# Kernel tuning notes

Measured on AMD Instinct MI355X. Metric: run time of the kernel, lower is better.

## Reference

```python
import jax, jax.numpy as jnp
import numpy as np

BIN_SIZE = 128
DIST_MULT = 0.1
CLIP_LOW = 0.0
EPS = 1e-6


def setup_inputs() -> dict:
    key = jax.random.key(0)
    k1, k2, k3, k4 = jax.random.split(key, 4)
    B, N = 8, 25600          # n_points multiple of bin_size=128 -> 200 bins
    D_MSG, D_NODE = 128, 256  # distance_dim, node feature dim
    MAX_BINS = 200
    x_msg = jax.random.normal(k1, (B, N, D_MSG), dtype=jnp.float32)
    x_node = jax.random.normal(k2, (B, N, D_NODE), dtype=jnp.float32)
    msk = jax.random.uniform(k3, (B, N)) < 0.9
    rotations = jax.random.normal(k4, (D_MSG, MAX_BINS // 2), dtype=jnp.float32)
    return {"x_msg": x_msg, "x_node": x_node, "msk": msk, "rotations": rotations}


def reference(x_msg, x_node, msk, rotations):
    B, N, _ = x_msg.shape
    n_bins = N // BIN_SIZE

    # LSH projection and binning
    mul = x_msg @ rotations[:, : max(1, n_bins // 2)]          # (B, N, n_bins/2)
    cmul = jnp.concatenate([mul, -mul], axis=-1)               # (B, N, n_bins)
    bin_idx = jnp.argmax(cmul, axis=-1) + jnp.where(~msk, n_bins - 1, 0)
    bins_split = jnp.argsort(bin_idx, axis=-1).reshape(B, n_bins, BIN_SIZE)

    # gather points into bins (batch_dims=1 gather)
    flat = bins_split.reshape(B, N)
    x_msg_b = jnp.take_along_axis(x_msg, flat[..., None], axis=1).reshape(B, n_bins, BIN_SIZE, -1)
    x_node_b = jnp.take_along_axis(x_node, flat[..., None], axis=1).reshape(B, n_bins, BIN_SIZE, -1)
    msk_f = msk.astype(x_msg.dtype)[..., None]                 # (B, N, 1)
    msk_b = jnp.take_along_axis(msk_f, flat[..., None], axis=1).reshape(B, n_bins, BIN_SIZE, 1)

    # NodePairGaussianKernel (l2 norm) within each bin
    x = x_msg_b * msk_b                                        # (B, nb, P, D)
    sq = jnp.sum(jnp.square(x), axis=-1)                       # (B, nb, P)
    gram = jnp.einsum('bkid,bkjd->bkij', x, x)                 # (B, nb, P, P)
    d = jnp.sqrt(jnp.maximum(sq[..., :, None] - 2.0 * gram + sq[..., None, :], EPS))
    dm = jnp.clip(jnp.exp(-DIST_MULT * d), CLIP_LOW, 1.0)[..., None]  # (B, nb, P, P, 1)

    # mask rows and columns
    dm = dm * msk_b[:, :, :, None, :] * msk_b[:, :, None, :, :]
    return bins_split, x_node_b, dm, msk_b
```

## Files before the change

kernel.cpp:

```cpp
#include <hip/hip_runtime.h>
#include <stdint.h>

typedef unsigned int uint32;

#define B 8
#define N 25600
#define DMSG 128
#define DNODE 256
#define NBINS 200
#define PBIN 128
#define NR 100
#define NPASS 4
#define JPP 25
#define NKEY 400
#define CH 256
#define NCHUNK 100
#define EPS 1e-6f
#define DISTM 0.1f

typedef short short8 __attribute__((ext_vector_type(8)));
typedef float floatx4 __attribute__((ext_vector_type(4)));

__device__ __forceinline__ unsigned short f2bf(float f) {
    uint32 u = __float_as_uint(f);
    u += 0x7fffu + ((u >> 16) & 1u);
    return (unsigned short)(u >> 16);
}

__global__ __launch_bounds__(256, 2) void k_bin(const float* __restrict__ xmsg,
                                                const int* __restrict__ msk,
                                                const float* __restrict__ rot,
                                                int* __restrict__ binidx,
                                                int* __restrict__ counts) {
    __shared__ float Xs[CH][36];
    __shared__ int hist[NKEY];
    const int tid = threadIdx.x;
    const int b = blockIdx.x / NCHUNK;
    const int chunk = blockIdx.x % NCHUNK;
    const int pbase = b * N + chunk * CH;

    double bestp = -1e300, bestn = -1e300;
    int bjp = 0, bjn = 0;

    for (int pass = 0; pass < NPASS; pass++) {
        double acc[JPP];
#pragma unroll
        for (int j = 0; j < JPP; j++) acc[j] = 0.0;

        for (int kc = 0; kc < 4; kc++) {
            __syncthreads();
#pragma unroll
            for (int i = 0; i < 8; i++) {
                int s = i * 256 + tid;
                int p = s >> 3, q = s & 7;
                float4 v = *(const float4*)(xmsg + (long)(pbase + p) * DMSG + kc * 32 + q * 4);
                *(float4*)&Xs[p][q * 4] = v;
            }
            __syncthreads();
#pragma unroll 1
            for (int k4 = 0; k4 < 8; k4++) {
                float4 xv = *(const float4*)&Xs[tid][k4 * 4];
#pragma unroll
                for (int c = 0; c < 4; c++) {
                    const double xk = (double)((c == 0) ? xv.x : (c == 1) ? xv.y : (c == 2) ? xv.z : xv.w);
                    const float* __restrict__ rrow = rot + (kc * 32 + k4 * 4 + c) * NR + pass * JPP;
#pragma unroll
                    for (int j = 0; j < JPP; j++) acc[j] = fma(xk, (double)rrow[j], acc[j]);
                }
            }
        }
#pragma unroll
        for (int j = 0; j < JPP; j++) {
            const int col = pass * JPP + j;
            if (acc[j] > bestp) { bestp = acc[j]; bjp = col; }
            if (-acc[j] > bestn) { bestn = -acc[j]; bjn = col; }
        }
    }
    const int bj = (bestp >= bestn) ? bjp : NR + bjn;
    const int m = msk[pbase + tid];
    const int bin = bj + (m ? 0 : (NBINS - 1));
    binidx[pbase + tid] = bin;

    for (int i = tid; i < NKEY; i += 256) hist[i] = 0;
    __syncthreads();
    atomicAdd(&hist[bin], 1);
    __syncthreads();
    for (int i = tid; i < NKEY; i += 256)
        counts[(b * NKEY + i) * NCHUNK + chunk] = hist[i];
}

__global__ void k_scan(int* __restrict__ counts) {
    const int b = blockIdx.x;
    const int base = b * (NKEY * NCHUNK);
    const int tot = NKEY * NCHUNK;
    const int seg = (tot + 255) / 256;
    const int tid = threadIdx.x;
    const int lo = tid * seg;
    const int hi = min(lo + seg, tot);
    int s = 0;
    for (int i = lo; i < hi; i++) s += counts[base + i];
    __shared__ int sums[256];
    sums[tid] = s;
    __syncthreads();
    if (tid == 0) {
        int run = 0;
        for (int i = 0; i < 256; i++) { int t = sums[i]; sums[i] = run; run += t; }
    }
    __syncthreads();
    int run = sums[tid];
    for (int i = lo; i < hi; i++) { int t = counts[base + i]; counts[base + i] = run; run += t; }
}

__global__ void k_scatter(const int* __restrict__ binidx, const int* __restrict__ counts,
                          int* __restrict__ perm, float* __restrict__ out0) {
    __shared__ int bins[CH];
    const int tid = threadIdx.x;
    const int b = blockIdx.x / NCHUNK;
    const int chunk = blockIdx.x % NCHUNK;
    const int n = chunk * CH + tid;
    const int bin = binidx[b * N + n];
    bins[tid] = bin;
    __syncthreads();
    int r = 0;
    for (int i = 0; i < CH; i++) {
        if (i < tid && bins[i] == bin) r++;
    }
    const int pos = counts[(b * NKEY + bin) * NCHUNK + chunk] + r;
    perm[b * N + pos] = n;
    out0[b * N + pos] = (float)n;
}

__global__ void k_gather(const float* __restrict__ xnode, const int* __restrict__ msk,
                         const int* __restrict__ perm, float* __restrict__ out1,
                         float* __restrict__ out3) {
    const int tid = threadIdx.x;
    const int wid = tid >> 6, lane = tid & 63;
    const int row = blockIdx.x * 4 + wid;
    const int b = row / N, pos = row % N;
    const int src = perm[b * N + pos];
    const float4* s4 = (const float4*)(xnode + (long)(b * N + src) * DNODE);
    float4* d4 = (float4*)(out1 + (long)row * DNODE);
    d4[lane] = s4[lane];
    if (lane == 0) out3[row] = msk[b * N + src] ? 1.0f : 0.0f;
}

__global__ void k_dm(const float* __restrict__ xmsg, const int* __restrict__ msk,
                     const int* __restrict__ perm, float* __restrict__ out2) {
    __shared__ unsigned short Xbf[PBIN][136];
    __shared__ float ssq[256];
    __shared__ float sq[PBIN];
    __shared__ float mm[PBIN];
    const int tid = threadIdx.x;
    const int b = blockIdx.x / NBINS;
    const int bin = blockIdx.x % NBINS;

    const int row = tid >> 1, half = tid & 1;
    const int src = perm[b * N + bin * PBIN + row];
    const float mf = msk[b * N + src] ? 1.0f : 0.0f;
    if (half == 0) mm[row] = mf;
    const float4* xp = (const float4*)(xmsg + (long)(b * N + src) * DMSG + half * 64);
    float ss = 0.f;
#pragma unroll
    for (int i = 0; i < 16; i++) {
        float4 v = xp[i];
        v.x *= mf; v.y *= mf; v.z *= mf; v.w *= mf;
        ss += v.x * v.x + v.y * v.y + v.z * v.z + v.w * v.w;
        uint2 pk;
        pk.x = (uint32)f2bf(v.x) | ((uint32)f2bf(v.y) << 16);
        pk.y = (uint32)f2bf(v.z) | ((uint32)f2bf(v.w) << 16);
        *(uint2*)&Xbf[row][half * 64 + i * 4] = pk;
    }
    ssq[tid] = ss;
    __syncthreads();
    if (tid < PBIN) sq[tid] = ssq[2 * tid] + ssq[2 * tid + 1];
    __syncthreads();

    const int w = tid >> 6, lane = tid & 63;
    const int lrow = lane & 15, quad = lane >> 4;

    short8 af[2][4];
#pragma unroll
    for (int t = 0; t < 2; t++) {
        int rr = (w * 2 + t) * 16 + lrow;
#pragma unroll
        for (int kk = 0; kk < 4; kk++)
            af[t][kk] = *(const short8*)&Xbf[rr][kk * 32 + quad * 8];
    }

    const long obase = (long)(b * NBINS + bin) * (PBIN * PBIN);
#pragma unroll 1
    for (int tc = 0; tc < 8; tc++) {
        const int cc = tc * 16 + lrow;
        short8 bf[4];
#pragma unroll
        for (int kk = 0; kk < 4; kk++)
            bf[kk] = *(const short8*)&Xbf[cc][kk * 32 + quad * 8];
        const float sqc = sq[cc];
        const float mc = mm[cc];
#pragma unroll
        for (int t = 0; t < 2; t++) {
            floatx4 acc = {0.f, 0.f, 0.f, 0.f};
#pragma unroll
            for (int kk = 0; kk < 4; kk++)
                acc = __builtin_amdgcn_mfma_f32_16x16x32_bf16(af[t][kk], bf[kk], acc, 0, 0, 0);
            const int rbase = (w * 2 + t) * 16 + quad * 4;
#pragma unroll
            for (int i = 0; i < 4; i++) {
                int rr = rbase + i;
                float val = sq[rr] + sqc - 2.f * acc[i];
                val = (rr == cc) ? EPS : fmaxf(val, EPS);
                float d = sqrtf(val);
                float e = fminf(__expf(-DISTM * d), 1.0f);
                out2[obase + (long)rr * PBIN + cc] = e * mm[rr] * mc;
            }
        }
    }
}

extern "C" void kernel_launch(void* const* d_in, const int* in_sizes, int n_in,
                              void* d_out, int out_size, void* d_ws, size_t ws_size,
                              hipStream_t stream) {
    const float* xmsg  = (const float*)d_in[0];
    const float* xnode = (const float*)d_in[1];
    const int*   msk   = (const int*)d_in[2];
    const float* rot   = (const float*)d_in[3];

    int* ws = (int*)d_ws;
    int* binidx = ws;
    int* counts = ws + B * N;
    int* perm   = ws + B * N + B * NKEY * NCHUNK;

    float* out0 = (float*)d_out;
    float* out1 = out0 + (long)B * N;
    float* out2 = out1 + (long)B * N * DNODE;
    float* out3 = out2 + (long)B * NBINS * PBIN * PBIN;

    k_bin<<<B * NCHUNK, 256, 0, stream>>>(xmsg, msk, rot, binidx, counts);
    k_scan<<<B, 256, 0, stream>>>(counts);
    k_scatter<<<B * NCHUNK, 256, 0, stream>>>(binidx, counts, perm, out0);
    k_gather<<<(B * N) / 4, 256, 0, stream>>>(xnode, msk, perm, out1, out3);
    k_dm<<<B * NBINS, 256, 0, stream>>>(xmsg, msk, perm, out2);
}
```

Measured before the change: 951.1 us.

## Compute LSH projections in fp32 with fp64 recheck for near-tie argmax

The binning kernel now computes all 100 projections in a single fp32 pass instead of four fp64 passes. It then finds the top two candidates across the positive and negative halves. When the margin between them is below a threshold, it recomputes only the close candidates in fp64 from global memory so the argmax still matches. This removes slow fp64 FMA throughput and the repeated reloading of the shared tile. In exchange, each thread now holds 100 live float accumulators, which raises register pressure, and some threads take a divergent fallback path.

```diff
diff --git a/kernel.cpp b/kernel.cpp
--- a/kernel.cpp
+++ b/kernel.cpp
@@ -10,8 +10,6 @@
 #define NBINS 200
 #define PBIN 128
 #define NR 100
-#define NPASS 4
-#define JPP 25
 #define NKEY 400
 #define CH 256
 #define NCHUNK 100
@@ -39,44 +37,80 @@
     const int chunk = blockIdx.x % NCHUNK;
     const int pbase = b * N + chunk * CH;
 
-    double bestp = -1e300, bestn = -1e300;
-    int bjp = 0, bjn = 0;
-
-    for (int pass = 0; pass < NPASS; pass++) {
-        double acc[JPP];
-#pragma unroll
-        for (int j = 0; j < JPP; j++) acc[j] = 0.0;
-
-        for (int kc = 0; kc < 4; kc++) {
-            __syncthreads();
-#pragma unroll
-            for (int i = 0; i < 8; i++) {
-                int s = i * 256 + tid;
-                int p = s >> 3, q = s & 7;
-                float4 v = *(const float4*)(xmsg + (long)(pbase + p) * DMSG + kc * 32 + q * 4);
-                *(float4*)&Xs[p][q * 4] = v;
+    float acc[NR];
+#pragma unroll
+    for (int j = 0; j < NR; j++) acc[j] = 0.f;
+
+#pragma unroll 1
+    for (int kc = 0; kc < 4; kc++) {
+        __syncthreads();
+#pragma unroll
+        for (int i = 0; i < 8; i++) {
+            int s = i * 256 + tid;
+            int p = s >> 3, q = s & 7;
+            float4 v = *(const float4*)(xmsg + (long)(pbase + p) * DMSG + kc * 32 + q * 4);
+            *(float4*)&Xs[p][q * 4] = v;
+        }
+        __syncthreads();
+#pragma unroll 1
+        for (int k4 = 0; k4 < 8; k4++) {
+            float4 xv = *(const float4*)&Xs[tid][k4 * 4];
+#pragma unroll
+            for (int c = 0; c < 4; c++) {
+                const float xk = (c == 0) ? xv.x : (c == 1) ? xv.y : (c == 2) ? xv.z : xv.w;
+                const float* __restrict__ rrow = rot + (kc * 32 + k4 * 4 + c) * NR;
+#pragma unroll
+                for (int jc = 0; jc < 4; jc++)
+#pragma unroll
+                    for (int j = 0; j < 25; j++)
+                        acc[jc * 25 + j] = fmaf(xk, rrow[jc * 25 + j], acc[jc * 25 + j]);
             }
-            __syncthreads();
-#pragma unroll 1
-            for (int k4 = 0; k4 < 8; k4++) {
-                float4 xv = *(const float4*)&Xs[tid][k4 * 4];
-#pragma unroll
-                for (int c = 0; c < 4; c++) {
-                    const double xk = (double)((c == 0) ? xv.x : (c == 1) ? xv.y : (c == 2) ? xv.z : xv.w);
-                    const float* __restrict__ rrow = rot + (kc * 32 + k4 * 4 + c) * NR + pass * JPP;
-#pragma unroll
-                    for (int j = 0; j < JPP; j++) acc[j] = fma(xk, (double)rrow[j], acc[j]);
-                }
-            }
-        }
-#pragma unroll
-        for (int j = 0; j < JPP; j++) {
-            const int col = pass * JPP + j;
-            if (acc[j] > bestp) { bestp = acc[j]; bjp = col; }
-            if (-acc[j] > bestn) { bestn = -acc[j]; bjn = col; }
-        }
-    }
-    const int bj = (bestp >= bestn) ? bjp : NR + bjn;
+        }
+    }
+
+    float m1 = -1e30f, m2 = -1e30f;
+    int i1 = 0;
+#pragma unroll
+    for (int j = 0; j < NR; j++) {
+        const float a = acc[j];
+        if (a > m1) { m2 = m1; m1 = a; i1 = j; }
+        else if (a > m2) { m2 = a; }
+    }
+#pragma unroll
+    for (int j = 0; j < NR; j++) {
+        const float a = -acc[j];
+        if (a > m1) { m2 = m1; m1 = a; i1 = NR + j; }
+        else if (a > m2) { m2 = a; }
+    }
+    int bj = i1;
+
+    const float THRESH = 0.02f;
+    if (m1 - m2 < THRESH) {
+        const float cut = m1 - THRESH;
+        unsigned long long cm0 = 0ull, cm1 = 0ull;
+#pragma unroll
+        for (int j = 0; j < 64; j++)
+            cm0 |= ((unsigned long long)(fmaxf(acc[j], -acc[j]) >= cut)) << j;
+#pragma unroll
+        for (int j = 64; j < NR; j++)
+            cm1 |= ((unsigned long long)(fmaxf(acc[j], -acc[j]) >= cut)) << (j - 64);
+
+        const float* __restrict__ xrow = xmsg + (long)(pbase + tid) * DMSG;
+        double bestp = -1e300, bestn = -1e300;
+        int bjp = 0, bjn = 0;
+        while (cm0 | cm1) {
+            int j;
+            if (cm0) { j = __ffsll(cm0) - 1; cm0 &= cm0 - 1; }
+            else     { j = 64 + __ffsll(cm1) - 1; cm1 &= cm1 - 1; }
+            double s = 0.0;
+            for (int k = 0; k < DMSG; k++)
+                s = fma((double)xrow[k], (double)rot[k * NR + j], s);
+            if (s > bestp)  { bestp = s;  bjp = j; }
+            if (-s > bestn) { bestn = -s; bjn = j; }
+        }
+        bj = (bestp >= bestn) ? bjp : NR + bjn;
+    }
+
     const int m = msk[pbase + tid];
     const int bin = bj + (m ? 0 : (NBINS - 1));
     binidx[pbase + tid] = bin;
```

New measurement: 812.3 us. -14.6%, faster.
